# Kernel tuning notes

Measured on AMD Instinct MI355X. Metric: run time of the kernel, lower is better.

The kernel has to match this reference:

```python
import jax, jax.numpy as jnp
import numpy as np

NUM_HEADS = 16
NEG = -10000000.0


def setup_inputs() -> dict:
    key = jax.random.key(0)
    k1, k2, k3 = jax.random.split(key, 3)
    B, N, C = 4, 2048, 1024
    inputs = jax.random.normal(k1, (B, N, C), dtype=jnp.float32)
    # learned params (xavier-ish scale)
    W_qkv = jax.random.normal(k2, (C, 3 * C), dtype=jnp.float32) * 0.02
    W_proj = jax.random.normal(k3, (C, C), dtype=jnp.float32) * 0.02
    b_proj = jnp.zeros((C,), dtype=jnp.float32)
    attn_mask = jnp.ones((N, N), dtype=jnp.int32)      # >0 means keep
    padding_mask = jnp.zeros((B, N), dtype=jnp.int32)  # >0 means mask out
    return {"inputs": inputs, "attn_mask": attn_mask, "padding_mask": padding_mask,
            "W_qkv": W_qkv, "W_proj": W_proj, "b_proj": b_proj}


def reference(inputs, attn_mask, padding_mask, W_qkv, W_proj, b_proj):
    B, N, C = inputs.shape
    H = NUM_HEADS
    d = C // H
    scale = d ** -0.5
    qkv = inputs @ W_qkv                                   # [B,N,3C]
    qkv = qkv.reshape(B, N, 3, H, d).transpose(2, 0, 3, 1, 4)  # [3,B,H,N,d]
    q, k, v = qkv[0], qkv[1], qkv[2]
    scores = jnp.einsum('bhqd,bhkd->bhqk', q, k) * scale   # [B,H,N,N]
    scores = jnp.where(attn_mask > 0, scores, NEG)
    pm = padding_mask[:, None, None, :]                    # [B,1,1,N]
    scores = jnp.where(pm > 0, NEG, scores)
    attn = jax.nn.softmax(scores, axis=-1)
    x = jnp.einsum('bhqk,bhkd->bhqd', attn, v)             # [B,H,N,d]
    x = x.swapaxes(1, 2).reshape(B, N, C)
    return x @ W_proj + b_proj
```

## Files before the change

kernel.cpp:

```cpp
#include <hip/hip_runtime.h>

#define NEG -10000000.0f
#define QSCALE 0.18033688011112042f

typedef __attribute__((ext_vector_type(8))) short bf16x8;
typedef __attribute__((ext_vector_type(4))) float f32x4;

static __device__ __forceinline__ short f2bf(float f) {
    unsigned int u = __float_as_uint(f);
    unsigned int r = (u + 0x7fffu + ((u >> 16) & 1u)) >> 16;
    return (short)r;
}

static __device__ __forceinline__ unsigned pack_bf16_2(float a, float b) {
    unsigned ua = __float_as_uint(a) + 0x8000u;
    unsigned ub = __float_as_uint(b) + 0x8000u;
    return __builtin_amdgcn_perm(ub, ua, 0x07060302u);
}

static __device__ __forceinline__ void async_cp16(const void* g, void* l) {
    __builtin_amdgcn_global_load_lds(
        (const __attribute__((address_space(1))) unsigned int*)g,
        (__attribute__((address_space(3))) unsigned int*)l, 16, 0, 0);
}

__global__ void cvt_bf16(const float* __restrict__ src, short* __restrict__ dst, int n4) {
    int i = blockIdx.x * blockDim.x + threadIdx.x;
    if (i < n4) {
        float4 v = reinterpret_cast<const float4*>(src)[i];
        short4 o;
        o.x = f2bf(v.x); o.y = f2bf(v.y); o.z = f2bf(v.z); o.w = f2bf(v.w);
        reinterpret_cast<short4*>(dst)[i] = o;
    }
}

__global__ void transpose_cvt(const float* __restrict__ src, short* __restrict__ dst,
                              int rows, int cols) {
    __shared__ float tile[32][33];
    int bx = blockIdx.x * 32;
    int by = blockIdx.y * 32;
    int tx = threadIdx.x & 31, ty = threadIdx.x >> 5;
    for (int j = 0; j < 4; ++j)
        tile[ty + j * 8][tx] = src[(size_t)(by + ty + j * 8) * cols + bx + tx];
    __syncthreads();
    for (int j = 0; j < 4; ++j)
        dst[(size_t)(bx + ty + j * 8) * rows + by + tx] = f2bf(tile[tx][ty + j * 8]);
}

__global__ void mask_flags(const int* __restrict__ attn_mask,
                           const int* __restrict__ padding, int* __restrict__ flags) {
    int blk = blockIdx.x;
    int tid = threadIdx.x;
    if (blk == 512) {
        if (tid < 128) {
            int b = tid >> 5, kt = tid & 31;
            int any = 0;
            for (int j = 0; j < 64; ++j) any |= (padding[b * 2048 + kt * 64 + j] > 0);
            flags[512 + tid] = any;
        }
        return;
    }
    int qt = blk >> 5, kt = blk & 31;
    __shared__ int blockok;
    if (tid == 0) blockok = 1;
    __syncthreads();
    int ok = 1;
    for (int j = 0; j < 32; ++j) {
        int idx = j * 256 + tid;
        int qr = qt * 128 + (idx >> 6);
        int kc = kt * 64 + (idx & 63);
        ok &= (attn_mask[(size_t)qr * 2048 + kc] != 0);
    }
    if (!ok) blockok = 0;
    __syncthreads();
    if (tid == 0) flags[blk] = blockok;
}

__global__ __launch_bounds__(256, 2) void gemm_bf16(
    const short* __restrict__ A, const short* __restrict__ Bt, int mode,
    short* __restrict__ q_ws, short* __restrict__ k_ws, short* __restrict__ v_ws,
    float* __restrict__ out, const float* __restrict__ bias) {
    const int K = 1024;
    __shared__ __align__(16) short smem[2][128][64];
    short (*As)[64] = smem[0];
    short (*Bs)[64] = smem[1];
    int tid = threadIdx.x, lane = tid & 63, w = tid >> 6;
    int wm = w & 1, wn = w >> 1;

    int nwg = gridDim.x * gridDim.y;
    int hw = blockIdx.y * gridDim.x + blockIdx.x;
    int logical = (hw & 7) * (nwg >> 3) + (hw >> 3);
    int bx = logical % gridDim.x, by = logical / gridDim.x;
    int m0 = by * 128, n0 = bx * 128;

    int col = lane & 15, quad = lane >> 4;
    int l8 = lane >> 3, j8 = lane & 7;

    f32x4 acc[4][4] = {};

    for (int k0 = 0; k0 < K; k0 += 64) {
        for (int c = 0; c < 4; ++c) {
            int rr = w * 32 + c * 8 + l8;
            int sw = (j8 ^ (rr & 7)) << 3;
            async_cp16(&A[(size_t)(m0 + rr) * K + k0 + sw], &As[w * 32 + c * 8][0]);
            async_cp16(&Bt[(size_t)(n0 + rr) * K + k0 + sw], &Bs[w * 32 + c * 8][0]);
        }
        __syncthreads();
        for (int ks = 0; ks < 2; ++ks) {
            bf16x8 af[4], bfr[4];
            for (int mt = 0; mt < 4; ++mt)
                af[mt] = *reinterpret_cast<const bf16x8*>(
                    &As[wm * 64 + mt * 16 + col][((ks * 4 + quad) ^ (col & 7)) << 3]);
            for (int nt = 0; nt < 4; ++nt)
                bfr[nt] = *reinterpret_cast<const bf16x8*>(
                    &Bs[wn * 64 + nt * 16 + col][((ks * 4 + quad) ^ (col & 7)) << 3]);
            for (int mt = 0; mt < 4; ++mt)
                for (int nt = 0; nt < 4; ++nt)
                    acc[mt][nt] = __builtin_amdgcn_mfma_f32_16x16x32_bf16(af[mt], bfr[nt], acc[mt][nt], 0, 0, 0);
        }
        __syncthreads();
    }

    short* L = &smem[0][0][0];

    if (mode == 0) {
        int which = n0 >> 10;
        int cb = n0 & 1023;
        int b = m0 >> 11, nb = m0 & 2047, hb = cb >> 6;
        if (which == 2) {
            for (int mt = 0; mt < 4; ++mt)
                for (int nt = 0; nt < 4; ++nt) {
                    int ml = wm * 64 + mt * 16 + quad * 4;
                    int cl = wn * 64 + nt * 16 + col;
                    int mp = (ml + 8 * cl) & 127;
                    short4 pk;
                    for (int r = 0; r < 4; ++r) ((short*)&pk)[r] = f2bf(acc[mt][nt][r]);
                    *reinterpret_cast<short4*>(&L[cl * 128 + mp]) = pk;
                }
            __syncthreads();
            for (int it = 0; it < 8; ++it) {
                int chunk = it * 256 + tid;
                int c = chunk >> 4, j = chunk & 15;
                int h = hb + (c >> 6), dd = c & 63;
                int4 val = *reinterpret_cast<const int4*>(&L[c * 128 + (((j + c) & 15) << 3)]);
                *reinterpret_cast<int4*>(
                    &v_ws[((size_t)((b * 16 + h) * 64 + dd)) * 2048 + nb + j * 8]) = val;
            }
        } else {
            short* dst = (which == 0) ? q_ws : k_ws;
            float scl = (which == 0) ? QSCALE : 1.0f;
            for (int mt = 0; mt < 4; ++mt)
                for (int nt = 0; nt < 4; ++nt)
                    for (int r = 0; r < 4; ++r) {
                        int ml = wm * 64 + mt * 16 + quad * 4 + r;
                        int cl = wn * 64 + nt * 16 + col;
                        L[ml * 128 + ((cl + 8 * ml) & 127)] = f2bf(acc[mt][nt][r] * scl);
                    }
            __syncthreads();
            for (int it = 0; it < 8; ++it) {
                int chunk = it * 256 + tid;
                int row = chunk >> 4, j = chunk & 15;
                int h = hb + (j >> 3), dd = (j & 7) * 8;
                int4 val = *reinterpret_cast<const int4*>(&L[row * 128 + (((j + row) & 15) << 3)]);
                *reinterpret_cast<int4*>(
                    &dst[((size_t)(b * 16 + h) * 2048 + nb + row) * 64 + dd]) = val;
            }
        }
    } else {
        float* Lf = reinterpret_cast<float*>(L);
        for (int half = 0; half < 2; ++half) {
            if (wm == half) {
                for (int mt = 0; mt < 4; ++mt)
                    for (int nt = 0; nt < 4; ++nt)
                        for (int r = 0; r < 4; ++r) {
                            int ml = mt * 16 + quad * 4 + r;
                            int cl = wn * 64 + nt * 16 + col;
                            Lf[ml * 128 + cl] = acc[mt][nt][r];
                        }
            }
            __syncthreads();
            for (int it = 0; it < 8; ++it) {
                int chunk = it * 256 + tid;
                int row = chunk >> 5, j = chunk & 31;
                float4 val = *reinterpret_cast<const float4*>(&Lf[row * 128 + j * 4]);
                float4 bv = *reinterpret_cast<const float4*>(&bias[n0 + j * 4]);
                val.x += bv.x; val.y += bv.y; val.z += bv.z; val.w += bv.w;
                *reinterpret_cast<float4*>(
                    &out[(size_t)(m0 + half * 64 + row) * 1024 + n0 + j * 4]) = val;
            }
            __syncthreads();
        }
    }
}

__global__ __launch_bounds__(512, 6) void flash_attn(
    const short* __restrict__ q_ws, const short* __restrict__ k_ws,
    const short* __restrict__ v_ws, const int* __restrict__ aflags,
    const int* __restrict__ pflags, const int* __restrict__ padding,
    const int* __restrict__ attn_mask, short* __restrict__ xb) {
    const int Nn = 2048, D = 64;
    __shared__ short QP[128][64];
    __shared__ short Ks[64][64];
    __shared__ short Vt[64][64];
    __shared__ __align__(16) float padb[64];

    int tid = threadIdx.x, lane = tid & 63, w = tid >> 6;
    int col = lane & 15, quad = lane >> 4;

    int hw = blockIdx.y * 16 + blockIdx.x;
    int logical = (hw & 7) * 128 + (hw >> 3);
    int bh = logical >> 4, qt = logical & 15;
    int b = bh >> 4, h = bh & 15;
    int q0 = qt * 128;

    int l8 = lane >> 3, j8 = lane & 7;

    unsigned amask = (unsigned)__ballot(aflags[qt * 32 + (lane & 31)] != 0);
    unsigned pmask = (unsigned)__ballot(pflags[b * 32 + (lane & 31)] != 0);

    for (int c = 0; c < 2; ++c) {
        int rr = w * 16 + c * 8 + l8;
        async_cp16(&q_ws[((size_t)bh * Nn + q0 + rr) * D + ((j8 ^ (rr & 7)) << 3)],
                   &QP[w * 16 + c * 8][0]);
    }
    __syncthreads();

    bf16x8 qf[2];
    for (int ks = 0; ks < 2; ++ks)
        qf[ks] = *reinterpret_cast<const bf16x8*>(
            &QP[w * 16 + col][((ks * 4 + quad) ^ (col & 7)) << 3]);

    f32x4 oacc[4] = {};
    f32x4 lacc = {};

    for (int kt = 0; kt < 32; ++kt) {
        int k0 = kt * 64;
        {
            int rr = w * 8 + l8;
            int sw = (j8 ^ (rr & 7)) << 3;
            async_cp16(&k_ws[((size_t)bh * Nn + k0 + rr) * D + sw], &Ks[w * 8][0]);
            async_cp16(&v_ws[((size_t)bh * D + rr) * Nn + k0 + sw], &Vt[w * 8][0]);
        }
        int pflag = (pmask >> kt) & 1;
        if (pflag && tid < 64) padb[tid] = (padding[b * Nn + k0 + tid] > 0) ? NEG : 0.f;
        __syncthreads();

        f32x4 sacc[4] = {};
        for (int ks = 0; ks < 2; ++ks) {
            bf16x8 kf[4];
            for (int mt = 0; mt < 4; ++mt)
                kf[mt] = *reinterpret_cast<const bf16x8*>(
                    &Ks[mt * 16 + col][((ks * 4 + quad) ^ (col & 7)) << 3]);
            __builtin_amdgcn_s_setprio(1);
            for (int mt = 0; mt < 4; ++mt)
                sacc[mt] = __builtin_amdgcn_mfma_f32_16x16x32_bf16(kf[mt], qf[ks], sacc[mt], 0, 0, 0);
            __builtin_amdgcn_s_setprio(0);
        }

        if (!((amask >> kt) & 1)) {
            int qr = q0 + w * 16 + col;
            for (int mt = 0; mt < 4; ++mt)
                for (int r = 0; r < 4; ++r) {
                    int kc = k0 + mt * 16 + quad * 4 + r;
                    if (attn_mask[(size_t)qr * Nn + kc] == 0) sacc[mt][r] = NEG;
                }
        }
        if (pflag) {
            for (int mt = 0; mt < 4; ++mt) {
                f32x4 pb = *reinterpret_cast<const f32x4*>(&padb[mt * 16 + quad * 4]);
                for (int r = 0; r < 4; ++r) sacc[mt][r] += pb[r];
            }
        }

        {
            int qrow = w * 16 + col;
            for (int mt = 0; mt < 4; ++mt) {
                f32x4 e;
                e[0] = __builtin_amdgcn_exp2f(sacc[mt][0]);
                e[1] = __builtin_amdgcn_exp2f(sacc[mt][1]);
                e[2] = __builtin_amdgcn_exp2f(sacc[mt][2]);
                e[3] = __builtin_amdgcn_exp2f(sacc[mt][3]);
                lacc += e;
                unsigned p0 = pack_bf16_2(e[0], e[1]);
                unsigned p1 = pack_bf16_2(e[2], e[3]);
                int chunk = (mt * 2 + (quad >> 1)) ^ (col & 7);
                *reinterpret_cast<uint2*>(&QP[qrow][(chunk << 3) + ((quad & 1) << 2)]) =
                    make_uint2(p0, p1);
            }
        }

        for (int ks = 0; ks < 2; ++ks) {
            bf16x8 pf, vf[4];
            pf = *reinterpret_cast<const bf16x8*>(
                &QP[w * 16 + col][((ks * 4 + quad) ^ (col & 7)) << 3]);
            for (int nt = 0; nt < 4; ++nt)
                vf[nt] = *reinterpret_cast<const bf16x8*>(
                    &Vt[nt * 16 + col][((ks * 4 + quad) ^ (col & 7)) << 3]);
            __builtin_amdgcn_s_setprio(1);
            for (int nt = 0; nt < 4; ++nt)
                oacc[nt] = __builtin_amdgcn_mfma_f32_16x16x32_bf16(pf, vf[nt], oacc[nt], 0, 0, 0);
            __builtin_amdgcn_s_setprio(0);
        }
        __syncthreads();
    }

    {
        float ls = lacc[0] + lacc[1] + lacc[2] + lacc[3];
        ls += __shfl_xor(ls, 16);
        ls += __shfl_xor(ls, 32);
        for (int r = 0; r < 4; ++r) {
            float lv = __shfl(ls, quad * 4 + r, 16);
            float inv = 1.f / lv;
            int n = q0 + w * 16 + quad * 4 + r;
            for (int nt = 0; nt < 4; ++nt) {
                int dd = nt * 16 + col;
                xb[((size_t)(b * Nn + n)) * 1024 + h * 64 + dd] = f2bf(oacc[nt][r] * inv);
            }
        }
    }
}

extern "C" void kernel_launch(void* const* d_in, const int* in_sizes, int n_in,
                              void* d_out, int out_size, void* d_ws, size_t ws_size,
                              hipStream_t stream) {
    const float* x        = (const float*)d_in[0];
    const int* attn_mask  = (const int*)d_in[1];
    const int* padding    = (const int*)d_in[2];
    const float* W_qkv    = (const float*)d_in[3];
    const float* W_proj   = (const float*)d_in[4];
    const float* b_proj   = (const float*)d_in[5];
    float* out            = (float*)d_out;

    char* ws = (char*)d_ws;
    short* Xb   = (short*)(ws);
    short* Wqt  = (short*)(ws + (16u << 20));
    short* Wpt  = (short*)(ws + (22u << 20));
    short* q_ws = (short*)(ws + (24u << 20));
    short* k_ws = (short*)(ws + (40u << 20));
    short* v_ws = (short*)(ws + (56u << 20));
    short* xbuf = (short*)(ws + (72u << 20));
    int*  flags = (int*)(ws + (88u << 20));

    cvt_bf16<<<8192, 256, 0, stream>>>(x, Xb, 8388608 / 4);
    transpose_cvt<<<dim3(3072 / 32, 1024 / 32), 256, 0, stream>>>(W_qkv, Wqt, 1024, 3072);
    transpose_cvt<<<dim3(1024 / 32, 1024 / 32), 256, 0, stream>>>(W_proj, Wpt, 1024, 1024);
    mask_flags<<<513, 256, 0, stream>>>(attn_mask, padding, flags);

    gemm_bf16<<<dim3(3072 / 128, 8192 / 128), 256, 0, stream>>>(
        Xb, Wqt, 0, q_ws, k_ws, v_ws, nullptr, nullptr);

    flash_attn<<<dim3(16, 64), 512, 0, stream>>>(
        q_ws, k_ws, v_ws, flags, flags + 512, padding, attn_mask, xbuf);

    gemm_bf16<<<dim3(1024 / 128, 8192 / 128), 256, 0, stream>>>(
        xbuf, Wpt, 1, nullptr, nullptr, nullptr, out, b_proj);
}
```

Baseline: 314.0 us.

## Use 32x32x16 MFMA in flash attention with 4 waves of 32 query rows

Flash attention now uses the 32x32x16 bf16 MFMA instead of 16x16x32, with each of 4 waves owning 32 query rows (256 threads per block instead of 512). The P matrix is kept in registers and rearranged with v_permlane32_swap, so it no longer round-trips through LDS before the PV multiply. The intent is fewer LDS reads per MFMA and less shared-memory traffic. The cost is more accumulator registers per wave and fewer waves per block, which may reduce occupancy and latency hiding.

```diff
diff --git a/kernel.cpp b/kernel.cpp
--- a/kernel.cpp
+++ b/kernel.cpp
@@ -5,6 +5,7 @@
 
 typedef __attribute__((ext_vector_type(8))) short bf16x8;
 typedef __attribute__((ext_vector_type(4))) float f32x4;
+typedef __attribute__((ext_vector_type(16))) float f32x16;
 
 static __device__ __forceinline__ short f2bf(float f) {
     unsigned int u = __float_as_uint(f);
@@ -193,7 +194,7 @@
     }
 }
 
-__global__ __launch_bounds__(512, 6) void flash_attn(
+__global__ __launch_bounds__(256, 4) void flash_attn(
     const short* __restrict__ q_ws, const short* __restrict__ k_ws,
     const short* __restrict__ v_ws, const int* __restrict__ aflags,
     const int* __restrict__ pflags, const int* __restrict__ padding,
@@ -205,7 +206,7 @@
     __shared__ __align__(16) float padb[64];
 
     int tid = threadIdx.x, lane = tid & 63, w = tid >> 6;
-    int col = lane & 15, quad = lane >> 4;
+    int c32 = lane & 31, hl = lane >> 5;
 
     int hw = blockIdx.y * 16 + blockIdx.x;
     int logical = (hw & 7) * 128 + (hw >> 3);
@@ -215,109 +216,109 @@
 
     int l8 = lane >> 3, j8 = lane & 7;
 
-    unsigned amask = (unsigned)__ballot(aflags[qt * 32 + (lane & 31)] != 0);
-    unsigned pmask = (unsigned)__ballot(pflags[b * 32 + (lane & 31)] != 0);
-
-    for (int c = 0; c < 2; ++c) {
-        int rr = w * 16 + c * 8 + l8;
+    unsigned amask = (unsigned)__ballot(aflags[qt * 32 + c32] != 0);
+    unsigned pmask = (unsigned)__ballot(pflags[b * 32 + c32] != 0);
+
+    for (int c = 0; c < 4; ++c) {
+        int rr = w * 32 + c * 8 + l8;
         async_cp16(&q_ws[((size_t)bh * Nn + q0 + rr) * D + ((j8 ^ (rr & 7)) << 3)],
-                   &QP[w * 16 + c * 8][0]);
+                   &QP[w * 32 + c * 8][0]);
     }
     __syncthreads();
 
-    bf16x8 qf[2];
-    for (int ks = 0; ks < 2; ++ks)
+    bf16x8 qf[4];
+    for (int ks = 0; ks < 4; ++ks)
         qf[ks] = *reinterpret_cast<const bf16x8*>(
-            &QP[w * 16 + col][((ks * 4 + quad) ^ (col & 7)) << 3]);
-
-    f32x4 oacc[4] = {};
-    f32x4 lacc = {};
+            &QP[w * 32 + c32][((2 * ks + hl) ^ (c32 & 7)) << 3]);
+
+    f32x16 oacc[2] = {};
+    f32x4 lac = {};
 
     for (int kt = 0; kt < 32; ++kt) {
         int k0 = kt * 64;
-        {
-            int rr = w * 8 + l8;
+        for (int c = 0; c < 2; ++c) {
+            int rr = w * 16 + c * 8 + l8;
             int sw = (j8 ^ (rr & 7)) << 3;
-            async_cp16(&k_ws[((size_t)bh * Nn + k0 + rr) * D + sw], &Ks[w * 8][0]);
-            async_cp16(&v_ws[((size_t)bh * D + rr) * Nn + k0 + sw], &Vt[w * 8][0]);
+            async_cp16(&k_ws[((size_t)bh * Nn + k0 + rr) * D + sw], &Ks[w * 16 + c * 8][0]);
+            async_cp16(&v_ws[((size_t)bh * D + rr) * Nn + k0 + sw], &Vt[w * 16 + c * 8][0]);
         }
         int pflag = (pmask >> kt) & 1;
         if (pflag && tid < 64) padb[tid] = (padding[b * Nn + k0 + tid] > 0) ? NEG : 0.f;
         __syncthreads();
 
-        f32x4 sacc[4] = {};
-        for (int ks = 0; ks < 2; ++ks) {
-            bf16x8 kf[4];
-            for (int mt = 0; mt < 4; ++mt)
-                kf[mt] = *reinterpret_cast<const bf16x8*>(
-                    &Ks[mt * 16 + col][((ks * 4 + quad) ^ (col & 7)) << 3]);
-            __builtin_amdgcn_s_setprio(1);
-            for (int mt = 0; mt < 4; ++mt)
-                sacc[mt] = __builtin_amdgcn_mfma_f32_16x16x32_bf16(kf[mt], qf[ks], sacc[mt], 0, 0, 0);
-            __builtin_amdgcn_s_setprio(0);
-        }
+        f32x16 sacc[2] = {};
+        __builtin_amdgcn_s_setprio(1);
+        for (int ks = 0; ks < 4; ++ks) {
+            bf16x8 kf0 = *reinterpret_cast<const bf16x8*>(
+                &Ks[c32][((2 * ks + hl) ^ (c32 & 7)) << 3]);
+            bf16x8 kf1 = *reinterpret_cast<const bf16x8*>(
+                &Ks[32 + c32][((2 * ks + hl) ^ (c32 & 7)) << 3]);
+            sacc[0] = __builtin_amdgcn_mfma_f32_32x32x16_bf16(kf0, qf[ks], sacc[0], 0, 0, 0);
+            sacc[1] = __builtin_amdgcn_mfma_f32_32x32x16_bf16(kf1, qf[ks], sacc[1], 0, 0, 0);
+        }
+        __builtin_amdgcn_s_setprio(0);
 
         if (!((amask >> kt) & 1)) {
-            int qr = q0 + w * 16 + col;
-            for (int mt = 0; mt < 4; ++mt)
-                for (int r = 0; r < 4; ++r) {
-                    int kc = k0 + mt * 16 + quad * 4 + r;
+            int qr = q0 + w * 32 + c32;
+            for (int mt = 0; mt < 2; ++mt)
+                for (int r = 0; r < 16; ++r) {
+                    int kc = k0 + mt * 32 + (r & 3) + 8 * (r >> 2) + 4 * hl;
                     if (attn_mask[(size_t)qr * Nn + kc] == 0) sacc[mt][r] = NEG;
                 }
         }
         if (pflag) {
-            for (int mt = 0; mt < 4; ++mt) {
-                f32x4 pb = *reinterpret_cast<const f32x4*>(&padb[mt * 16 + quad * 4]);
-                for (int r = 0; r < 4; ++r) sacc[mt][r] += pb[r];
-            }
-        }
-
-        {
-            int qrow = w * 16 + col;
-            for (int mt = 0; mt < 4; ++mt) {
-                f32x4 e;
-                e[0] = __builtin_amdgcn_exp2f(sacc[mt][0]);
-                e[1] = __builtin_amdgcn_exp2f(sacc[mt][1]);
-                e[2] = __builtin_amdgcn_exp2f(sacc[mt][2]);
-                e[3] = __builtin_amdgcn_exp2f(sacc[mt][3]);
-                lacc += e;
-                unsigned p0 = pack_bf16_2(e[0], e[1]);
-                unsigned p1 = pack_bf16_2(e[2], e[3]);
-                int chunk = (mt * 2 + (quad >> 1)) ^ (col & 7);
-                *reinterpret_cast<uint2*>(&QP[qrow][(chunk << 3) + ((quad & 1) << 2)]) =
-                    make_uint2(p0, p1);
-            }
-        }
-
-        for (int ks = 0; ks < 2; ++ks) {
-            bf16x8 pf, vf[4];
-            pf = *reinterpret_cast<const bf16x8*>(
-                &QP[w * 16 + col][((ks * 4 + quad) ^ (col & 7)) << 3]);
-            for (int nt = 0; nt < 4; ++nt)
-                vf[nt] = *reinterpret_cast<const bf16x8*>(
-                    &Vt[nt * 16 + col][((ks * 4 + quad) ^ (col & 7)) << 3]);
+            for (int mt = 0; mt < 2; ++mt)
+                for (int r = 0; r < 16; ++r)
+                    sacc[mt][r] += padb[mt * 32 + (r & 3) + 8 * (r >> 2) + 4 * hl];
+        }
+
+        for (int mt = 0; mt < 2; ++mt)
+            for (int r = 0; r < 16; ++r)
+                sacc[mt][r] = __builtin_amdgcn_exp2f(sacc[mt][r]);
+        for (int mt = 0; mt < 2; ++mt)
+            for (int r = 0; r < 4; ++r) {
+                lac[0] += sacc[mt][4 * r + 0];
+                lac[1] += sacc[mt][4 * r + 1];
+                lac[2] += sacc[mt][4 * r + 2];
+                lac[3] += sacc[mt][4 * r + 3];
+            }
+
+        for (int ks2 = 0; ks2 < 4; ++ks2) {
+            int mt = ks2 >> 1, g = (ks2 & 1) * 8;
+            unsigned a  = pack_bf16_2(sacc[mt][g + 0], sacc[mt][g + 1]);
+            unsigned a2 = pack_bf16_2(sacc[mt][g + 2], sacc[mt][g + 3]);
+            unsigned bb = pack_bf16_2(sacc[mt][g + 4], sacc[mt][g + 5]);
+            unsigned b2 = pack_bf16_2(sacc[mt][g + 6], sacc[mt][g + 7]);
+            asm("v_permlane32_swap_b32 %0, %1" : "+v"(a), "+v"(bb));
+            asm("v_permlane32_swap_b32 %0, %1" : "+v"(a2), "+v"(b2));
+            union { unsigned u[4]; bf16x8 v; } pu;
+            pu.u[0] = a; pu.u[1] = a2; pu.u[2] = bb; pu.u[3] = b2;
+            bf16x8 v0 = *reinterpret_cast<const bf16x8*>(
+                &Vt[c32][((2 * ks2 + hl) ^ (c32 & 7)) << 3]);
+            bf16x8 v1 = *reinterpret_cast<const bf16x8*>(
+                &Vt[32 + c32][((2 * ks2 + hl) ^ (c32 & 7)) << 3]);
             __builtin_amdgcn_s_setprio(1);
-            for (int nt = 0; nt < 4; ++nt)
-                oacc[nt] = __builtin_amdgcn_mfma_f32_16x16x32_bf16(pf, vf[nt], oacc[nt], 0, 0, 0);
+            oacc[0] = __builtin_amdgcn_mfma_f32_32x32x16_bf16(v0, pu.v, oacc[0], 0, 0, 0);
+            oacc[1] = __builtin_amdgcn_mfma_f32_32x32x16_bf16(v1, pu.v, oacc[1], 0, 0, 0);
             __builtin_amdgcn_s_setprio(0);
         }
         __syncthreads();
     }
 
-    {
-        float ls = lacc[0] + lacc[1] + lacc[2] + lacc[3];
-        ls += __shfl_xor(ls, 16);
-        ls += __shfl_xor(ls, 32);
-        for (int r = 0; r < 4; ++r) {
-            float lv = __shfl(ls, quad * 4 + r, 16);
-            float inv = 1.f / lv;
-            int n = q0 + w * 16 + quad * 4 + r;
-            for (int nt = 0; nt < 4; ++nt) {
-                int dd = nt * 16 + col;
-                xb[((size_t)(b * Nn + n)) * 1024 + h * 64 + dd] = f2bf(oacc[nt][r] * inv);
-            }
-        }
-    }
+    float ls = lac[0] + lac[1] + lac[2] + lac[3];
+    ls += __shfl_xor(ls, 32);
+    float inv = 1.f / ls;
+    int qrow = b * Nn + q0 + w * 32 + c32;
+    for (int nt = 0; nt < 2; ++nt)
+        for (int g = 0; g < 4; ++g) {
+            short4 pk4;
+            ((short*)&pk4)[0] = f2bf(oacc[nt][4 * g + 0] * inv);
+            ((short*)&pk4)[1] = f2bf(oacc[nt][4 * g + 1] * inv);
+            ((short*)&pk4)[2] = f2bf(oacc[nt][4 * g + 2] * inv);
+            ((short*)&pk4)[3] = f2bf(oacc[nt][4 * g + 3] * inv);
+            *reinterpret_cast<short4*>(
+                &xb[(size_t)qrow * 1024 + h * 64 + nt * 32 + 8 * g + 4 * hl]) = pk4;
+        }
 }
 
 extern "C" void kernel_launch(void* const* d_in, const int* in_sizes, int n_in,
@@ -349,7 +350,7 @@
     gemm_bf16<<<dim3(3072 / 128, 8192 / 128), 256, 0, stream>>>(
         Xb, Wqt, 0, q_ws, k_ws, v_ws, nullptr, nullptr);
 
-    flash_attn<<<dim3(16, 64), 512, 0, stream>>>(
+    flash_attn<<<dim3(16, 64), 256, 0, stream>>>(
         q_ws, k_ws, v_ws, flags, flags + 512, padding, attn_mask, xbuf);
 
     gemm_bf16<<<dim3(1024 / 128, 8192 / 128), 256, 0, stream>>>(
```

Result: no change. 310.5 us (-1.1%).
